# Optimization experiments

Hardware: AMD Instinct MI355X
Metric: run time of the kernel (lower is better)

Reference implementation:

```python
import jax, jax.numpy as jnp
import numpy as np

ALPHA = 2.0    # ATan surrogate sharpness
V_TH = 1.0     # LIF firing threshold
TAU = 2.0      # LIF membrane time constant
BN_EPS = 1e-5
NUM_HEADS = 8

@jax.custom_vjp
def spike(u):
    return (u >= 0.0).astype(u.dtype)

def _spike_fwd(u):
    return spike(u), u

def _spike_bwd(u, g):
    s = (jnp.pi / 2.0) * ALPHA * u
    return (g * (ALPHA / 2.0) / (1.0 + s * s),)

spike.defvjp(_spike_fwd, _spike_bwd)

def lif(x):
    # x: (T, ...) -> binary spikes, multi-step LIF with hard reset
    def step(mem, xt):
        mem = mem + (xt - mem) / TAU
        s = spike(mem - V_TH)
        return mem * (1.0 - s), s
    _, out = jax.lax.scan(step, jnp.zeros_like(x[0]), x)
    return out

def bn_eval(y, bn):
    g, be, m, v = bn[0], bn[1], bn[2], bn[3]  # each (C,)
    return (y - m) * jax.lax.rsqrt(v + BN_EPS) * g + be

def linear_bn_lif(x, W, b, bn):
    # x: (T,B,N,C); W: (C_out, C_in) torch convention
    y = jnp.einsum('tbnc,dc->tbnd', x, W) + b
    return lif(bn_eval(y, bn))

def setup_inputs() -> dict:
    key = jax.random.key(0)
    ks = jax.random.split(key, 6)
    T, B, N, C = 4, 8, 1024, 512
    scale = 1.0 / np.sqrt(C)
    x = jax.random.normal(ks[0], (T, B, N, C), dtype=jnp.float32)
    Wq = jax.random.normal(ks[1], (C, C), dtype=jnp.float32) * scale
    Wk = jax.random.normal(ks[2], (C, C), dtype=jnp.float32) * scale
    Wv = jax.random.normal(ks[3], (C, C), dtype=jnp.float32) * scale
    Wp = jax.random.normal(ks[4], (C, C), dtype=jnp.float32) * scale
    zeros = jnp.zeros((C,), dtype=jnp.float32)
    ones = jnp.ones((C,), dtype=jnp.float32)
    # bn_params[l] = (gamma, beta, running_mean, running_var) for q_bn,k_bn,v_bn,proj_bn
    bn_one = jnp.stack([ones, zeros, zeros, ones])  # (4, C)
    bn_params = jnp.tile(bn_one[None], (4, 1, 1))   # (4, 4, C)
    return {"x": x, "Wq": Wq, "bq": zeros, "Wk": Wk, "bk": zeros,
            "Wv": Wv, "bv": zeros, "Wp": Wp, "bp": zeros, "bn_params": bn_params}

def reference(x, Wq, bq, Wk, bk, Wv, bv, Wp, bp, bn_params):
    T, B, N, C = x.shape
    H = NUM_HEADS
    D = C // H
    q = linear_bn_lif(x, Wq, bq, bn_params[0])
    k = linear_bn_lif(x, Wk, bk, bn_params[1])
    v = linear_bn_lif(x, Wv, bv, bn_params[2])
    # (T,B,N,C) -> (T,B,H,N,D)
    q = q.reshape(T, B, N, H, D).transpose(0, 1, 3, 2, 4)
    k = k.reshape(T, B, N, H, D).transpose(0, 1, 3, 2, 4)
    v = v.reshape(T, B, N, H, D).transpose(0, 1, 3, 2, 4)
    # attention_linear variant: kv = (k^T @ v) / n; y = q @ kv
    # SparseMatmul's tile-sparsity fallback computes the same dense matmul math.
    kv = jnp.einsum('tbhnd,tbhne->tbhde', k, v) / float(N)
    y = jnp.einsum('tbhnd,tbhde->tbhne', q, kv)
    y = y.transpose(0, 1, 3, 2, 4).reshape(T, B, N, C)
    y = lif(y)  # attn_lif
    # final projection: proj -> proj_bn -> proj_lif
    y = jnp.einsum('tbnc,dc->tbnd', y, Wp) + bp
    y = bn_eval(y, bn_params[3])
    y = lif(y)  # proj_lif
    return y
```

## Files before the change

kernel.cpp:

```cpp
#include <hip/hip_runtime.h>
#include <hip/hip_bf16.h>

constexpr int T_ = 4, B_ = 8, N_ = 1024, C_ = 512, H_ = 8, D_ = 64;
constexpr int M_ = 8192;
constexpr int MT_ = 32768;
constexpr int K_ = 512;

#define TAU_INV 0.5f
#define V_TH    1.0f
#define BN_EPS  1e-5f

typedef float v2f __attribute__((ext_vector_type(2)));
typedef float v4f __attribute__((ext_vector_type(4)));

__device__ __forceinline__ void ld4(const float* p, float* d) {
  const float4 v = *(const float4*)p;
  d[0] = v.x; d[1] = v.y; d[2] = v.z; d[3] = v.w;
}
__device__ __forceinline__ void ld4(const __hip_bfloat16* p, float* d) {
  const ushort4 u = *(const ushort4*)p;
  d[0] = __bfloat162float(*(const __hip_bfloat16*)&u.x);
  d[1] = __bfloat162float(*(const __hip_bfloat16*)&u.y);
  d[2] = __bfloat162float(*(const __hip_bfloat16*)&u.z);
  d[3] = __bfloat162float(*(const __hip_bfloat16*)&u.w);
}
__device__ __forceinline__ void ld4p(const float* p, v2f& lo, v2f& hi) {
  union { v4f v; v2f h[2]; } u;
  u.v = *(const v4f*)p;
  lo = u.h[0]; hi = u.h[1];
}
__device__ __forceinline__ void ld4p(const __hip_bfloat16* p, v2f& lo, v2f& hi) {
  const ushort4 u = *(const ushort4*)p;
  lo[0] = __bfloat162float(*(const __hip_bfloat16*)&u.x);
  lo[1] = __bfloat162float(*(const __hip_bfloat16*)&u.y);
  hi[0] = __bfloat162float(*(const __hip_bfloat16*)&u.z);
  hi[1] = __bfloat162float(*(const __hip_bfloat16*)&u.w);
}
__device__ __forceinline__ void ld8bf(const __hip_bfloat16* p, float* d) {
  union { uint4 u; ushort s[8]; } q;
  q.u = *(const uint4*)p;
#pragma unroll
  for (int j = 0; j < 8; ++j)
    d[j] = __bfloat162float(*(const __hip_bfloat16*)&q.s[j]);
}
__device__ __forceinline__ void st4(__hip_bfloat16* p, const float* s) {
  ushort4 u;
  *(__hip_bfloat16*)&u.x = __float2bfloat16(s[0]);
  *(__hip_bfloat16*)&u.y = __float2bfloat16(s[1]);
  *(__hip_bfloat16*)&u.z = __float2bfloat16(s[2]);
  *(__hip_bfloat16*)&u.w = __float2bfloat16(s[3]);
  *(ushort4*)p = u;
}
__device__ __forceinline__ void st4(float* p, const float* s) {
  *(float4*)p = make_float4(s[0], s[1], s[2], s[3]);
}

__device__ __forceinline__ void pk_fma_lo(v2f& acc, const v2f a, const v2f b) {
  asm("v_pk_fma_f32 %0, %1, %2, %0 op_sel:[0,0,0] op_sel_hi:[0,1,1]"
      : "+v"(acc) : "v"(a), "v"(b));
}
__device__ __forceinline__ void pk_fma_hi(v2f& acc, const v2f a, const v2f b) {
  asm("v_pk_fma_f32 %0, %1, %2, %0 op_sel:[1,0,0] op_sel_hi:[1,1,1]"
      : "+v"(acc) : "v"(a), "v"(b));
}

__device__ __forceinline__ void dma16(const void* g, void* l) {
  __builtin_amdgcn_global_load_lds(
      (const __attribute__((address_space(1))) unsigned int*)g,
      (__attribute__((address_space(3))) unsigned int*)l, 16, 0, 0);
}

struct WPtrs { const float* W[4]; };

__global__ __launch_bounds__(256) void transpose_w(WPtrs wp, float* __restrict__ Wt)
{
  __shared__ float tile[32][33];
  const int w = blockIdx.z;
  const float* __restrict__ W = wp.W[w];
  float* __restrict__ dst = Wt + (size_t)w * K_ * C_;
  const int k0 = blockIdx.x * 32, d0 = blockIdx.y * 32;
  const int tx = threadIdx.x, ty = threadIdx.y;
#pragma unroll
  for (int i = 0; i < 32; i += 8)
    tile[ty + i][tx] = W[(size_t)(d0 + ty + i) * K_ + k0 + tx];
  __syncthreads();
#pragma unroll
  for (int i = 0; i < 32; i += 8)
    dst[(size_t)(k0 + ty + i) * C_ + d0 + tx] = tile[tx][ty + i];
}

__global__ __launch_bounds__(256) void transpose_x(
    const float* __restrict__ x, float* __restrict__ XT)
{
  __shared__ float tile[32][132];
  const int bk = blockIdx.x * 32, bm = blockIdx.y * 32;
  const int tx = threadIdx.x & 31, ty = threadIdx.x >> 5;
#pragma unroll
  for (int t = 0; t < T_; ++t)
#pragma unroll
    for (int i = 0; i < 4; ++i) {
      const int m = ty + 8 * i;
      tile[tx][m * 4 + t] = x[((size_t)t * M_ + bm + m) * K_ + bk + tx];
    }
  __syncthreads();
  const int k = threadIdx.x >> 3, q = threadIdx.x & 7;
#pragma unroll
  for (int u = 0; u < 4; ++u)
    st4(&XT[(size_t)(bk + k) * MT_ + bm * 4 + q * 16 + u * 4],
        &tile[k][q * 16 + u * 4]);
}

template <typename TIn, typename TOut>
struct GArgs {
  const TIn* AT;
  const float* Wt[3];
  const float* bias[3];
  const float* bn[3];
  TOut* S[3];
};

template <typename TIn, typename TOut, int NH>
__global__ __launch_bounds__(256, 3) void gemm_lif(GArgs<TIn, TOut> args)
{
  constexpr int BK = 16;
  constexpr int BN = 64 * NH;
  constexpr bool BF = (sizeof(TIn) == 2);
  __shared__ __align__(16) TIn  As[BK * 128];
  __shared__ __align__(16) float Bs[BK * BN];

  const int z = blockIdx.z;
  const TIn*   __restrict__ AT   = args.AT;
  const float* __restrict__ Wt   = args.Wt[z];
  const float* __restrict__ bias = args.bias[z];
  const float* __restrict__ bnp  = args.bn[z];
  TOut*        __restrict__ S    = args.S[z];

  const int tid  = threadIdx.x;
  const int lane = tid & 63;
  const int wave = __builtin_amdgcn_readfirstlane(tid >> 6);
  const int tx = tid & 15, ty = tid >> 4;
  const int bm_m = blockIdx.y * 32;
  const int bm4  = bm_m * 4;
  const int bn0  = blockIdx.x * BN;

  v2f acc[2][NH][4][2];
#pragma unroll
  for (int g = 0; g < 2; ++g)
#pragma unroll
    for (int h = 0; h < NH; ++h)
#pragma unroll
      for (int i = 0; i < 4; ++i)
#pragma unroll
        for (int jp = 0; jp < 2; ++jp) { acc[g][h][i][jp][0] = 0.0f; acc[g][h][i][jp][1] = 0.0f; }

#pragma unroll 1
  for (int k0 = 0; k0 < K_; k0 += BK) {
    if constexpr (!BF) {
#pragma unroll
      for (int c = 0; c < 2; ++c) {
        const int ins = wave * 2 + c;
        const int kk = ins * 2 + (lane >> 5);
        dma16(AT + (size_t)(k0 + kk) * MT_ + bm4 + (lane & 31) * 4,
              (void*)((float*)As + ins * 256));
      }
    } else {
      const int kk = wave * 4 + (lane >> 4);
      dma16(AT + (size_t)(k0 + kk) * MT_ + bm4 + (lane & 15) * 8,
            (void*)((TIn*)As + wave * 512));
    }
#pragma unroll
    for (int c = 0; c < NH; ++c) {
      const int ins = wave * NH + c;
      int kk, col;
      if constexpr (NH == 4) { kk = ins;                     col = lane * 4; }
      else                   { kk = ins * 2 + (lane >> 5);   col = (lane & 31) * 4; }
      dma16(Wt + (size_t)(k0 + kk) * C_ + bn0 + col,
            (void*)(Bs + ins * 256));
    }
    __syncthreads();

#pragma unroll
    for (int kk = 0; kk < BK; ++kk) {
      v2f aL[2], aH[2], bL[NH], bH[NH];
#pragma unroll
      for (int g = 0; g < 2; ++g)
        ld4p((const TIn*)As + kk * 128 + ty * 4 + 64 * g, aL[g], aH[g]);
#pragma unroll
      for (int h = 0; h < NH; ++h)
        ld4p(Bs + kk * BN + tx * 4 + 64 * h, bL[h], bH[h]);
#pragma unroll
      for (int g = 0; g < 2; ++g)
#pragma unroll
        for (int h = 0; h < NH; ++h) {
          pk_fma_lo(acc[g][h][0][0], aL[g], bL[h]);
          pk_fma_lo(acc[g][h][0][1], aL[g], bH[h]);
          pk_fma_hi(acc[g][h][1][0], aL[g], bL[h]);
          pk_fma_hi(acc[g][h][1][1], aL[g], bH[h]);
          pk_fma_lo(acc[g][h][2][0], aH[g], bL[h]);
          pk_fma_lo(acc[g][h][2][1], aH[g], bH[h]);
          pk_fma_hi(acc[g][h][3][0], aH[g], bL[h]);
          pk_fma_hi(acc[g][h][3][1], aH[g], bH[h]);
        }
    }
    __syncthreads();
  }

#pragma unroll
  for (int h = 0; h < NH; ++h) {
    const int d = bn0 + tx * 4 + 64 * h;
    float bi[4], gg[4], be[4], mu[4], vv[4];
    ld4(&bias[d], bi);
    ld4(&bnp[d], gg);
    ld4(&bnp[C_ + d], be);
    ld4(&bnp[2 * C_ + d], mu);
    ld4(&bnp[3 * C_ + d], vv);
    float inv[4];
#pragma unroll
    for (int j = 0; j < 4; ++j) inv[j] = 1.0f / sqrtf(vv[j] + BN_EPS);
#pragma unroll
    for (int g = 0; g < 2; ++g) {
      const int m = bm_m + ty + 16 * g;
      float sv[4][4];
#pragma unroll
      for (int j = 0; j < 4; ++j) {
        float mm = 0.0f;
#pragma unroll
        for (int t = 0; t < 4; ++t) {
          float y = acc[g][h][t][j >> 1][j & 1] + bi[j];
          y = (y - mu[j]) * inv[j] * gg[j] + be[j];
          float m2 = mm + (y - mm) * TAU_INV;
          float s = (m2 - V_TH >= 0.0f) ? 1.0f : 0.0f;
          sv[t][j] = s;
          mm = (s != 0.0f) ? 0.0f : m2;
        }
      }
#pragma unroll
      for (int t = 0; t < 4; ++t)
        st4(&S[((size_t)t * M_ + m) * C_ + d], sv[t]);
    }
  }
}

__global__ __launch_bounds__(256) void kv_kernel(
    const __hip_bfloat16* __restrict__ Kk,
    const __hip_bfloat16* __restrict__ V,
    float* __restrict__ kvpT)
{
  __shared__ __align__(16) __hip_bfloat16 Ks[64 * 64];
  __shared__ __align__(16) __hip_bfloat16 Vs[64 * 64];
  const int tid  = threadIdx.x;
  const int lane = tid & 63;
  const int w    = __builtin_amdgcn_readfirstlane(tid >> 6);
  const int h = blockIdx.x, b = blockIdx.y, t = blockIdx.z;
  const size_t base = ((size_t)(t * B_ + b) * N_) * C_ + (size_t)h * D_;
  const int d0 = (lane >> 3) * 8;
  const int e0 = (lane & 7) * 8;

  float acc[8][8];
#pragma unroll
  for (int i = 0; i < 8; ++i)
#pragma unroll
    for (int j = 0; j < 8; ++j) acc[i][j] = 0.0f;

  for (int nc = 0; nc < N_; nc += 64) {
#pragma unroll
    for (int c = 0; c < 2; ++c) {
      const int ins = w * 2 + c;
      const int row = ins * 8 + (lane >> 3);
      const int ch  = lane & 7;
      dma16(Kk + base + (size_t)(nc + row) * C_ + ch * 8,
            (void*)(Ks + ins * 512));
      dma16(V  + base + (size_t)(nc + row) * C_ + ch * 8,
            (void*)(Vs + ins * 512));
    }
    __syncthreads();
#pragma unroll
    for (int s = 0; s < 16; ++s) {
      const int nn = w * 16 + s;
      float a[8], bb[8];
      ld8bf(Ks + nn * 64 + d0, a);
      ld8bf(Vs + nn * 64 + e0, bb);
#pragma unroll
      for (int i = 0; i < 8; ++i)
#pragma unroll
        for (int j = 0; j < 8; ++j) acc[i][j] += a[i] * bb[j];
    }
    __syncthreads();
  }

  float* dst = kvpT + ((((size_t)t * B_ + b) * H_ + h) * 4 + w) * (size_t)(D_ * D_);
#pragma unroll
  for (int j = 0; j < 8; ++j) {
    float tmp[8];
#pragma unroll
    for (int i = 0; i < 8; ++i) tmp[i] = acc[i][j];
    st4(&dst[(e0 + j) * D_ + d0], tmp);
    st4(&dst[(e0 + j) * D_ + d0 + 4], tmp + 4);
  }
}

__device__ __forceinline__ unsigned bfpair(unsigned bits, int j, int half) {
  const unsigned p = (bits >> (j * 4 + half * 2)) & 3u;
  return ((p & 1u) ? 0x3F80u : 0u) | ((p & 2u) ? 0x3F800000u : 0u);
}

__global__ __launch_bounds__(256, 2) void attn_y(
    const __hip_bfloat16* __restrict__ Q,
    const float* __restrict__ kvpT,
    __hip_bfloat16* __restrict__ AT)
{
  __shared__ __align__(16) __hip_bfloat16 Qs[128 * 64];
  __shared__ __align__(16) float KVs[64][68];
  const int tid  = threadIdx.x;
  const int lane = tid & 63;
  const int w    = __builtin_amdgcn_readfirstlane(tid >> 6);
  const int n0 = blockIdx.x * 128;
  const int h  = blockIdx.y, b = blockIdx.z;
  const int ng = lane & 15;
  const int e0 = w * 16 + (lane >> 4) * 4;

  float mem[8][4];
  unsigned svb[8];
#pragma unroll
  for (int i = 0; i < 8; ++i) {
    svb[i] = 0u;
#pragma unroll
    for (int j = 0; j < 4; ++j) mem[i][j] = 0.0f;
  }

#pragma unroll
  for (int t = 0; t < T_; ++t) {
    if (t) __syncthreads();
#pragma unroll
    for (int c = 0; c < 4; ++c) {
      const int ins = w * 4 + c;
      const int row = ins * 8 + (lane >> 3);
      const int ch  = (lane & 7) ^ (ins & 7);
      dma16(Q + (size_t)(t * M_ + b * N_ + n0 + row) * C_ + h * D_ + ch * 8,
            (void*)(Qs + ins * 512));
    }
    const float* kp = kvpT + (((size_t)t * B_ + b) * H_ + h) * 4 * (size_t)(D_ * D_);
#pragma unroll
    for (int g = 0; g < 4; ++g) {
      const int cell = tid * 16 + g * 4;
      const float4 v0 = *(const float4*)(kp + cell);
      const float4 v1 = *(const float4*)(kp + 4096 + cell);
      const float4 v2 = *(const float4*)(kp + 8192 + cell);
      const float4 v3 = *(const float4*)(kp + 12288 + cell);
      float sum[4] = { v0.x + v1.x + v2.x + v3.x, v0.y + v1.y + v2.y + v3.y,
                       v0.z + v1.z + v2.z + v3.z, v0.w + v1.w + v2.w + v3.w };
      st4(&KVs[cell >> 6][cell & 63], sum);
    }
    __syncthreads();

    float acc[8][4];
#pragma unroll
    for (int i = 0; i < 8; ++i)
#pragma unroll
      for (int j = 0; j < 4; ++j) acc[i][j] = 0.0f;
#pragma unroll 2
    for (int dc = 0; dc < 8; ++dc) {
      float bb[4][8];
#pragma unroll
      for (int j = 0; j < 4; ++j) {
        ld4(&KVs[e0 + j][dc * 8], bb[j]);
        ld4(&KVs[e0 + j][dc * 8 + 4], bb[j] + 4);
      }
#pragma unroll
      for (int i = 0; i < 8; ++i) {
        float a[8];
        ld8bf(Qs + (ng * 8 + i) * 64 + ((dc ^ (ng & 7)) * 8), a);
#pragma unroll
        for (int dd = 0; dd < 8; ++dd)
#pragma unroll
          for (int j = 0; j < 4; ++j)
            acc[i][j] += a[dd] * bb[j][dd];
      }
    }

#pragma unroll
    for (int i = 0; i < 8; ++i)
#pragma unroll
      for (int j = 0; j < 4; ++j) {
        const float y = acc[i][j] * 0.0009765625f;
        const float m2 = mem[i][j] + (y - mem[i][j]) * TAU_INV;
        const float s = (m2 - V_TH >= 0.0f) ? 1.0f : 0.0f;
        if (s != 0.0f) svb[i] |= 1u << (j * 4 + t);
        mem[i][j] = (s != 0.0f) ? 0.0f : m2;
      }
  }

  const size_t mbase = ((size_t)b * N_ + n0 + ng * 8) * 4;
#pragma unroll
  for (int j = 0; j < 4; ++j) {
    __hip_bfloat16* dst = AT + (size_t)(h * D_ + e0 + j) * MT_ + mbase;
#pragma unroll
    for (int p = 0; p < 4; ++p) {
      uint4 u;
      u.x = bfpair(svb[2 * p],     j, 0);
      u.y = bfpair(svb[2 * p],     j, 1);
      u.z = bfpair(svb[2 * p + 1], j, 0);
      u.w = bfpair(svb[2 * p + 1], j, 1);
      *(uint4*)(dst + p * 8) = u;
    }
  }
}

extern "C" void kernel_launch(void* const* d_in, const int* in_sizes, int n_in,
                              void* d_out, int out_size, void* d_ws, size_t ws_size,
                              hipStream_t stream)
{
  const float* x   = (const float*)d_in[0];
  const float* Wq  = (const float*)d_in[1];
  const float* bq  = (const float*)d_in[2];
  const float* Wk  = (const float*)d_in[3];
  const float* bk  = (const float*)d_in[4];
  const float* Wv  = (const float*)d_in[5];
  const float* bv  = (const float*)d_in[6];
  const float* Wp  = (const float*)d_in[7];
  const float* bp  = (const float*)d_in[8];
  const float* bnp = (const float*)d_in[9];
  float* out = (float*)d_out;

  char* ws = (char*)d_ws;
  float* XT = (float*)ws;  ws += (size_t)K_ * MT_ * sizeof(float);
  float* Wt = (float*)ws;  ws += (size_t)4 * K_ * C_ * sizeof(float);
  __hip_bfloat16* q_s = (__hip_bfloat16*)ws; ws += (size_t)MT_ * C_ * 2;
  __hip_bfloat16* k_s = (__hip_bfloat16*)ws; ws += (size_t)MT_ * C_ * 2;
  __hip_bfloat16* v_s = (__hip_bfloat16*)ws; ws += (size_t)MT_ * C_ * 2;
  __hip_bfloat16* aT = (__hip_bfloat16*)XT;
  float* kvpT = (float*)((char*)XT + (size_t)32 * 1024 * 1024);

  WPtrs wp; wp.W[0] = Wq; wp.W[1] = Wk; wp.W[2] = Wv; wp.W[3] = Wp;
  transpose_w<<<dim3(K_ / 32, C_ / 32, 4), dim3(32, 8), 0, stream>>>(wp, Wt);
  transpose_x<<<dim3(K_ / 32, M_ / 32), 256, 0, stream>>>(x, XT);

  GArgs<float, __hip_bfloat16> qa;
  qa.AT = XT;
  qa.Wt[0] = Wt; qa.Wt[1] = Wt + (size_t)K_ * C_; qa.Wt[2] = Wt + (size_t)2 * K_ * C_;
  qa.bias[0] = bq; qa.bias[1] = bk; qa.bias[2] = bv;
  qa.bn[0] = bnp + 0 * 4 * C_;
  qa.bn[1] = bnp + 1 * 4 * C_;
  qa.bn[2] = bnp + 2 * 4 * C_;
  qa.S[0] = q_s; qa.S[1] = k_s; qa.S[2] = v_s;
  gemm_lif<float, __hip_bfloat16, 4>
      <<<dim3(C_ / 256, M_ / 32, 3), 256, 0, stream>>>(qa);

  kv_kernel<<<dim3(H_, B_, T_), 256, 0, stream>>>(k_s, v_s, kvpT);
  attn_y<<<dim3(N_ / 128, H_, B_), 256, 0, stream>>>(q_s, kvpT, aT);

  GArgs<__hip_bfloat16, float> pa;
  pa.AT = aT;
  pa.Wt[0] = Wt + (size_t)3 * K_ * C_;
  pa.bias[0] = bp;
  pa.bn[0] = bnp + 3 * 4 * C_;
  pa.S[0] = out;
  gemm_lif<__hip_bfloat16, float, 2>
      <<<dim3(C_ / 128, M_ / 32, 1), 256, 0, stream>>>(pa);
}
```

Before: 987.7 us.

## Split kv reduction across N quarters with atomic accumulation

The k^T·v kernel now launches four times as many blocks, each covering a quarter of the sequence. Every wave atomically adds its partial 64x64 product into a single zeroed kv buffer, replacing the four per-wave partial buffers. The memset and atomics add traffic, but the change raises parallelism from 256 blocks and lets attn_y load one buffer instead of summing four. Because float atomics land in varying order, the summation order is nondeterministic, which could flip spikes that sit near the threshold.

After: 1.387 ms. 1.4x slower.

```diff
diff --git a/kernel.cpp b/kernel.cpp
--- a/kernel.cpp
+++ b/kernel.cpp
@@ -244,14 +244,15 @@
 __global__ __launch_bounds__(256) void kv_kernel(
     const __hip_bfloat16* __restrict__ Kk,
     const __hip_bfloat16* __restrict__ V,
-    float* __restrict__ kvpT)
+    float* __restrict__ kvT)
 {
   __shared__ __align__(16) __hip_bfloat16 Ks[64 * 64];
   __shared__ __align__(16) __hip_bfloat16 Vs[64 * 64];
   const int tid  = threadIdx.x;
   const int lane = tid & 63;
   const int w    = __builtin_amdgcn_readfirstlane(tid >> 6);
-  const int h = blockIdx.x, b = blockIdx.y, t = blockIdx.z;
+  const int h = blockIdx.x, b = blockIdx.y;
+  const int t = blockIdx.z >> 2, nq = blockIdx.z & 3;
   const size_t base = ((size_t)(t * B_ + b) * N_) * C_ + (size_t)h * D_;
   const int d0 = (lane >> 3) * 8;
   const int e0 = (lane & 7) * 8;
@@ -262,7 +263,7 @@
 #pragma unroll
     for (int j = 0; j < 8; ++j) acc[i][j] = 0.0f;
 
-  for (int nc = 0; nc < N_; nc += 64) {
+  for (int nc = nq * 256; nc < nq * 256 + 256; nc += 64) {
 #pragma unroll
     for (int c = 0; c < 2; ++c) {
       const int ins = w * 2 + c;
@@ -288,15 +289,12 @@
     __syncthreads();
   }
 
-  float* dst = kvpT + ((((size_t)t * B_ + b) * H_ + h) * 4 + w) * (size_t)(D_ * D_);
-#pragma unroll
-  for (int j = 0; j < 8; ++j) {
-    float tmp[8];
-#pragma unroll
-    for (int i = 0; i < 8; ++i) tmp[i] = acc[i][j];
-    st4(&dst[(e0 + j) * D_ + d0], tmp);
-    st4(&dst[(e0 + j) * D_ + d0 + 4], tmp + 4);
-  }
+  float* dst = kvT + (((size_t)t * B_ + b) * H_ + h) * (size_t)(D_ * D_);
+#pragma unroll
+  for (int j = 0; j < 8; ++j)
+#pragma unroll
+    for (int i = 0; i < 8; ++i)
+      atomicAdd(&dst[(e0 + j) * D_ + d0 + i], acc[i][j]);
 }
 
 __device__ __forceinline__ unsigned bfpair(unsigned bits, int j, int half) {
@@ -306,7 +304,7 @@
 
 __global__ __launch_bounds__(256, 2) void attn_y(
     const __hip_bfloat16* __restrict__ Q,
-    const float* __restrict__ kvpT,
+    const float* __restrict__ kvT,
     __hip_bfloat16* __restrict__ AT)
 {
   __shared__ __align__(16) __hip_bfloat16 Qs[128 * 64];
@@ -339,17 +337,12 @@
       dma16(Q + (size_t)(t * M_ + b * N_ + n0 + row) * C_ + h * D_ + ch * 8,
             (void*)(Qs + ins * 512));
     }
-    const float* kp = kvpT + (((size_t)t * B_ + b) * H_ + h) * 4 * (size_t)(D_ * D_);
+    const float* kp = kvT + (((size_t)t * B_ + b) * H_ + h) * (size_t)(D_ * D_);
 #pragma unroll
     for (int g = 0; g < 4; ++g) {
       const int cell = tid * 16 + g * 4;
       const float4 v0 = *(const float4*)(kp + cell);
-      const float4 v1 = *(const float4*)(kp + 4096 + cell);
-      const float4 v2 = *(const float4*)(kp + 8192 + cell);
-      const float4 v3 = *(const float4*)(kp + 12288 + cell);
-      float sum[4] = { v0.x + v1.x + v2.x + v3.x, v0.y + v1.y + v2.y + v3.y,
-                       v0.z + v1.z + v2.z + v3.z, v0.w + v1.w + v2.w + v3.w };
-      st4(&KVs[cell >> 6][cell & 63], sum);
+      st4(&KVs[cell >> 6][cell & 63], (const float*)&v0);
     }
     __syncthreads();
 
@@ -429,7 +422,7 @@
   __hip_bfloat16* k_s = (__hip_bfloat16*)ws; ws += (size_t)MT_ * C_ * 2;
   __hip_bfloat16* v_s = (__hip_bfloat16*)ws; ws += (size_t)MT_ * C_ * 2;
   __hip_bfloat16* aT = (__hip_bfloat16*)XT;
-  float* kvpT = (float*)((char*)XT + (size_t)32 * 1024 * 1024);
+  float* kvT = (float*)((char*)XT + (size_t)32 * 1024 * 1024);
 
   WPtrs wp; wp.W[0] = Wq; wp.W[1] = Wk; wp.W[2] = Wv; wp.W[3] = Wp;
   transpose_w<<<dim3(K_ / 32, C_ / 32, 4), dim3(32, 8), 0, stream>>>(wp, Wt);
@@ -446,8 +439,9 @@
   gemm_lif<float, __hip_bfloat16, 4>
       <<<dim3(C_ / 256, M_ / 32, 3), 256, 0, stream>>>(qa);
 
-  kv_kernel<<<dim3(H_, B_, T_), 256, 0, stream>>>(k_s, v_s, kvpT);
-  attn_y<<<dim3(N_ / 128, H_, B_), 256, 0, stream>>>(q_s, kvpT, aT);
+  hipMemsetAsync(kvT, 0, (size_t)T_ * B_ * H_ * D_ * D_ * sizeof(float), stream);
+  kv_kernel<<<dim3(H_, B_, T_ * 4), 256, 0, stream>>>(k_s, v_s, kvT);
+  attn_y<<<dim3(N_ / 128, H_, B_), 256, 0, stream>>>(q_s, kvT, aT);
 
   GArgs<__hip_bfloat16, float> pa;
   pa.AT = aT;
```
